# Kernel optimization log

Measured on AMD Instinct MI355X. Metric: run time of the kernel, lower is better.

## Reference

```python
import jax, jax.numpy as jnp
import numpy as np

N_NODES = 100000
N_EDGES = 500000
D = 256
EPS = 0.1  # GIN epsilon applied on self-loop relation


def setup_inputs() -> dict:
    key = jax.random.key(0)
    ks = jax.random.split(key, 9)
    return {
        "x": jax.random.normal(ks[0], (N_NODES, D), dtype=jnp.float32),
        "W_self": jax.random.normal(ks[1], (D, D), dtype=jnp.float32) * 0.05,
        "W_r1": jax.random.normal(ks[2], (D, D), dtype=jnp.float32) * 0.05,
        "W_r2": jax.random.normal(ks[3], (D, D), dtype=jnp.float32) * 0.05,
        "bias": jax.random.normal(ks[4], (D,), dtype=jnp.float32) * 0.05,
        "src1": jax.random.randint(ks[5], (N_EDGES,), 0, N_NODES, dtype=jnp.int32),
        "dst1": jax.random.randint(ks[6], (N_EDGES,), 0, N_NODES, dtype=jnp.int32),
        "src2": jax.random.randint(ks[7], (N_EDGES,), 0, N_NODES, dtype=jnp.int32),
        "dst2": jax.random.randint(ks[8], (N_EDGES,), 0, N_NODES, dtype=jnp.int32),
    }


def reference(x, W_self, W_r1, W_r2, bias, src1, dst1, src2, dst2):
    # self-loop relation: features scaled by (1+eps); one self-loop edge per node
    # so copy_u + sum delivers each node exactly its own message.
    h = (1.0 + EPS) * (x @ W_self)
    # regular relations: per-node message = x @ W, gathered along src edges,
    # scatter-summed at dst (DGL fn.copy_u + fn.sum, cross-etype 'sum' reducer).
    msg1 = x @ W_r1
    h = h + jax.ops.segment_sum(msg1[src1], dst1, num_segments=N_NODES)
    msg2 = x @ W_r2
    h = h + jax.ops.segment_sum(msg2[src2], dst2, num_segments=N_NODES)
    # bias + activation, then second activation (applied twice in original);
    # mlp/batch_norm are None, dropout is identity in eval.
    h = jax.nn.relu(h + bias)
    h = jax.nn.relu(h)
    return h
```

## Files before the change

kernel.cpp:

```cpp
#include <hip/hip_runtime.h>

#define N_NODES 100000
#define N_EDGES 500000
#define D 256
#define CAP 32

typedef __bf16 bf16x8 __attribute__((ext_vector_type(8)));
typedef float  f32x4  __attribute__((ext_vector_type(4)));

#define GLDS(gp, lp) \
    __builtin_amdgcn_global_load_lds((const __attribute__((address_space(1))) void*)(gp), \
                                     (__attribute__((address_space(3))) void*)(lp), 16, 0, 0)

__device__ __forceinline__ unsigned short f2bf(float f) {
    unsigned int u = __float_as_uint(f);
    u += 0x7fffu + ((u >> 16) & 1u);
    return (unsigned short)(u >> 16);
}
__device__ __forceinline__ float bf2f(unsigned short b) {
    return __uint_as_float(((unsigned int)b) << 16);
}

#define CONV_B   12500
#define PW_B     768
#define BKT_B    3907
#define PREP_GRID (CONV_B + PW_B + BKT_B)

__global__ __launch_bounds__(256) void prep_kernel(
    const float* __restrict__ x, unsigned short* __restrict__ xb,
    const float* __restrict__ Ws, const float* __restrict__ W1,
    const float* __restrict__ W2, unsigned short* __restrict__ Wt,
    const int* __restrict__ src1, const int* __restrict__ dst1,
    const int* __restrict__ src2, const int* __restrict__ dst2,
    int* __restrict__ cnt1, int* __restrict__ cnt2,
    int* __restrict__ bkt1, int* __restrict__ bkt2)
{
    const int b = blockIdx.x;
    const int tid = threadIdx.x;
    if (b < CONV_B) {
        size_t i = ((size_t)b * 256 + tid) * 8;
        if (i >= (size_t)N_NODES * D) return;
        float4 a = *(const float4*)(x + i);
        float4 c = *(const float4*)(x + i + 4);
        union { unsigned short s[8]; uint4 u; } o;
        o.s[0] = f2bf(a.x); o.s[1] = f2bf(a.y); o.s[2] = f2bf(a.z); o.s[3] = f2bf(a.w);
        o.s[4] = f2bf(c.x); o.s[5] = f2bf(c.y); o.s[6] = f2bf(c.z); o.s[7] = f2bf(c.w);
        *(uint4*)(xb + i) = o.u;
    } else if (b < CONV_B + PW_B) {
        int idx = (b - CONV_B) * 256 + tid;
        int k = idx >> 8;
        int n = idx & (D - 1);
        const float* W = (k < D) ? Ws : (k < 2 * D ? W1 : W2);
        float scale = (k < D) ? 1.1f : 1.0f;
        Wt[(size_t)n * (3 * D) + k] = f2bf(W[(size_t)(k & (D - 1)) * D + n] * scale);
    } else {
        int e = (b - CONV_B - PW_B) * 256 + tid;
        if (e >= 2 * N_EDGES) return;
        const int* src; const int* dst; int* cnt; int* bkt; int ei;
        if (e < N_EDGES) { src = src1; dst = dst1; cnt = cnt1; bkt = bkt1; ei = e; }
        else             { src = src2; dst = dst2; cnt = cnt2; bkt = bkt2; ei = e - N_EDGES; }
        int s = src[ei], d = dst[ei];
        int pos = atomicAdd(&cnt[d], 1);
        if (pos < CAP) bkt[d * CAP + pos] = s;
    }
}

__global__ __launch_bounds__(256) void gather_kernel(
    const unsigned short* __restrict__ xb,
    const int* __restrict__ cnt1, const int* __restrict__ cnt2,
    const int* __restrict__ bkt1, const int* __restrict__ bkt2,
    unsigned short* __restrict__ xa1, unsigned short* __restrict__ xa2)
{
    long long gid = (long long)blockIdx.x * blockDim.x + threadIdx.x;
    int node = (int)(gid >> 6);
    int lane = (int)(gid & 63);
    if (node >= N_NODES) return;

    int c1 = cnt1[node]; if (c1 > CAP) c1 = CAP;
    int c2 = cnt2[node]; if (c2 > CAP) c2 = CAP;

    int sid1 = (lane < c1) ? bkt1[(size_t)node * CAP + lane] : 0;
    int sid2 = (lane < c2) ? bkt2[(size_t)node * CAP + lane] : 0;

    ushort4 v1[8], v2[8];
    #pragma unroll
    for (int t = 0; t < 8; ++t) {
        int s = __shfl(sid1, t);
        v1[t] = *(const ushort4*)(xb + (size_t)s * D + lane * 4);
    }
    #pragma unroll
    for (int t = 0; t < 8; ++t) {
        int s = __shfl(sid2, t);
        v2[t] = *(const ushort4*)(xb + (size_t)s * D + lane * 4);
    }

    float a10 = 0.f, a11 = 0.f, a12 = 0.f, a13 = 0.f;
    float a20 = 0.f, a21 = 0.f, a22 = 0.f, a23 = 0.f;
    #pragma unroll
    for (int t = 0; t < 8; ++t) {
        if (t < c1) {
            a10 += bf2f(v1[t].x); a11 += bf2f(v1[t].y);
            a12 += bf2f(v1[t].z); a13 += bf2f(v1[t].w);
        }
        if (t < c2) {
            a20 += bf2f(v2[t].x); a21 += bf2f(v2[t].y);
            a22 += bf2f(v2[t].z); a23 += bf2f(v2[t].w);
        }
    }
    for (int e = 8; e < c1; ++e) {
        int s = __shfl(sid1, e);
        ushort4 v = *(const ushort4*)(xb + (size_t)s * D + lane * 4);
        a10 += bf2f(v.x); a11 += bf2f(v.y); a12 += bf2f(v.z); a13 += bf2f(v.w);
    }
    for (int e = 8; e < c2; ++e) {
        int s = __shfl(sid2, e);
        ushort4 v = *(const ushort4*)(xb + (size_t)s * D + lane * 4);
        a20 += bf2f(v.x); a21 += bf2f(v.y); a22 += bf2f(v.z); a23 += bf2f(v.w);
    }

    ushort4 o1, o2;
    o1.x = f2bf(a10); o1.y = f2bf(a11); o1.z = f2bf(a12); o1.w = f2bf(a13);
    o2.x = f2bf(a20); o2.y = f2bf(a21); o2.z = f2bf(a22); o2.w = f2bf(a23);
    *(ushort4*)(xa1 + (size_t)node * D + lane * 4) = o1;
    *(ushort4*)(xa2 + (size_t)node * D + lane * 4) = o2;
}

__global__ __launch_bounds__(512) void gemm_kernel(
    const unsigned short* __restrict__ xb,
    const unsigned short* __restrict__ xa1,
    const unsigned short* __restrict__ xa2,
    const unsigned short* __restrict__ Wt,
    const float* __restrict__ bias, float* __restrict__ out)
{
    __shared__ unsigned short Alds[128 * 32];
    __shared__ unsigned short Blds[256 * 32];

    const int tid  = threadIdx.x;
    const int lane = tid & 63;
    const int wave = tid >> 6;
    const int quad = lane >> 4;
    const int l15  = lane & 15;
    const int m0 = blockIdx.x * 128;
    const int wm = (wave >> 2) * 64;
    const int wn = (wave & 3) * 64;

    const unsigned short* Aseg[3] = {xb, xa1, xa2};

    f32x4 acc[4][4] = {};

    for (int kt = 0; kt < 24; ++kt) {
        const int seg = kt >> 3;
        const int ko  = (kt & 7) * 32;
        const unsigned short* __restrict__ A = Aseg[seg];

        {
            int row = tid >> 2, kq = tid & 3;
            int m = m0 + row;
            if (m >= N_NODES) m = N_NODES - 1;
            GLDS(A + (size_t)m * D + ko + kq * 8, Alds + tid * 8);
        }
        {
            int n = tid >> 2, kq = tid & 3;
            GLDS(Wt + (size_t)n * (3 * D) + kt * 32 + kq * 8, Blds + tid * 8);
        }
        {
            int t2 = tid + 512;
            int n = t2 >> 2, kq = t2 & 3;
            GLDS(Wt + (size_t)n * (3 * D) + kt * 32 + kq * 8, Blds + t2 * 8);
        }
        __syncthreads();

        bf16x8 af[4], bfr[4];
        #pragma unroll
        for (int i = 0; i < 4; ++i) {
            af[i]  = *(const bf16x8*)(Alds + (wm + i * 16 + l15) * 32 + quad * 8);
            bfr[i] = *(const bf16x8*)(Blds + (wn + i * 16 + l15) * 32 + quad * 8);
        }
        #pragma unroll
        for (int i = 0; i < 4; ++i)
            #pragma unroll
            for (int j = 0; j < 4; ++j)
                acc[i][j] = __builtin_amdgcn_mfma_f32_16x16x32_bf16(
                    af[i], bfr[j], acc[i][j], 0, 0, 0);
        __syncthreads();
    }

    #pragma unroll
    for (int j = 0; j < 4; ++j) {
        int col = wn + j * 16 + l15;
        float bj = bias[col];
        #pragma unroll
        for (int i = 0; i < 4; ++i) {
            int rb = m0 + wm + i * 16 + quad * 4;
            #pragma unroll
            for (int r = 0; r < 4; ++r) {
                int m = rb + r;
                if (m < N_NODES)
                    out[(size_t)m * D + col] = fmaxf(acc[i][j][r] + bj, 0.f);
            }
        }
    }
}

extern "C" void kernel_launch(void* const* d_in, const int* in_sizes, int n_in,
                              void* d_out, int out_size, void* d_ws, size_t ws_size,
                              hipStream_t stream) {
    const float* x    = (const float*)d_in[0];
    const float* Ws   = (const float*)d_in[1];
    const float* W1   = (const float*)d_in[2];
    const float* W2   = (const float*)d_in[3];
    const float* bias = (const float*)d_in[4];
    const int* src1   = (const int*)d_in[5];
    const int* dst1   = (const int*)d_in[6];
    const int* src2   = (const int*)d_in[7];
    const int* dst2   = (const int*)d_in[8];
    float* out = (float*)d_out;

    char* p = (char*)d_ws;
    unsigned short* xb  = (unsigned short*)p; p += (size_t)N_NODES * D * 2;
    unsigned short* xa1 = (unsigned short*)p; p += (size_t)N_NODES * D * 2;
    unsigned short* xa2 = (unsigned short*)p; p += (size_t)N_NODES * D * 2;
    int* cnt1 = (int*)p; p += (size_t)N_NODES * 4;
    int* cnt2 = (int*)p; p += (size_t)N_NODES * 4;
    int* bkt1 = (int*)p; p += (size_t)N_NODES * CAP * 4;
    int* bkt2 = (int*)p; p += (size_t)N_NODES * CAP * 4;
    unsigned short* Wt = (unsigned short*)p;

    hipMemsetAsync(cnt1, 0, (size_t)2 * N_NODES * 4, stream);

    prep_kernel<<<PREP_GRID, 256, 0, stream>>>(
        x, xb, Ws, W1, W2, Wt, src1, dst1, src2, dst2, cnt1, cnt2, bkt1, bkt2);

    {
        long long total = (long long)N_NODES * 64;
        gather_kernel<<<(int)((total + 255) / 256), 256, 0, stream>>>(
            xb, cnt1, cnt2, bkt1, bkt2, xa1, xa2);
    }
    {
        gemm_kernel<<<(N_NODES + 127) / 128, 512, 0, stream>>>(
            xb, xa1, xa2, Wt, bias, out);
    }
}
```

Before: 446.8 us.

## Interleave prep work per wave, split gather by relation, use nontemporal stores

The prep kernel now assigns work per wave in interleaved groups of 22 (16 convert, 5 bucket, 1 weight-transpose waves), so the bandwidth-bound conversion overlaps with the latency-bound atomic bucketing instead of running them as separate block ranges. The gather kernel launches one wave per (node, relation) pair instead of one per node, doubling the wave count and halving per-wave registers to raise occupancy and memory-level parallelism. Stores of the aggregated features and of the final output use nontemporal hints to reduce cache pollution. The costs are more total waves doing the same index loads, and nontemporal writes for xa1/xa2 may evict data the gemm would otherwise find in cache.

After: 403.9 us. 9.6% less time.

```diff
diff --git a/kernel.cpp b/kernel.cpp
--- a/kernel.cpp
+++ b/kernel.cpp
@@ -7,6 +7,7 @@
 
 typedef __bf16 bf16x8 __attribute__((ext_vector_type(8)));
 typedef float  f32x4  __attribute__((ext_vector_type(4)));
+typedef unsigned int u32x2 __attribute__((ext_vector_type(2)));
 
 #define GLDS(gp, lp) \
     __builtin_amdgcn_global_load_lds((const __attribute__((address_space(1))) void*)(gp), \
@@ -21,10 +22,7 @@
     return __uint_as_float(((unsigned int)b) << 16);
 }
 
-#define CONV_B   12500
-#define PW_B     768
-#define BKT_B    3907
-#define PREP_GRID (CONV_B + PW_B + BKT_B)
+#define PREP_BLOCKS 17188
 
 __global__ __launch_bounds__(256) void prep_kernel(
     const float* __restrict__ x, unsigned short* __restrict__ xb,
@@ -35,33 +33,42 @@
     int* __restrict__ cnt1, int* __restrict__ cnt2,
     int* __restrict__ bkt1, int* __restrict__ bkt2)
 {
-    const int b = blockIdx.x;
-    const int tid = threadIdx.x;
-    if (b < CONV_B) {
-        size_t i = ((size_t)b * 256 + tid) * 8;
-        if (i >= (size_t)N_NODES * D) return;
+    const int wid  = blockIdx.x * 4 + (threadIdx.x >> 6);
+    const int lane = threadIdx.x & 63;
+    const int group = wid / 22;
+    const int pos   = wid - group * 22;
+
+    if (pos < 16) {
+        int cw = group * 16 + pos;
+        if (cw >= 50000) return;
+        size_t i = (size_t)cw * 512 + (size_t)lane * 8;
         float4 a = *(const float4*)(x + i);
         float4 c = *(const float4*)(x + i + 4);
         union { unsigned short s[8]; uint4 u; } o;
         o.s[0] = f2bf(a.x); o.s[1] = f2bf(a.y); o.s[2] = f2bf(a.z); o.s[3] = f2bf(a.w);
         o.s[4] = f2bf(c.x); o.s[5] = f2bf(c.y); o.s[6] = f2bf(c.z); o.s[7] = f2bf(c.w);
         *(uint4*)(xb + i) = o.u;
-    } else if (b < CONV_B + PW_B) {
-        int idx = (b - CONV_B) * 256 + tid;
+    } else if (pos < 21) {
+        int bw = group * 5 + (pos - 16);
+        int e = bw * 64 + lane;
+        if (e >= 2 * N_EDGES) return;
+        bool r2 = (e >= N_EDGES);
+        const int* src = r2 ? src2 : src1;
+        const int* dst = r2 ? dst2 : dst1;
+        int* cnt = r2 ? cnt2 : cnt1;
+        int* bkt = r2 ? bkt2 : bkt1;
+        int ei = r2 ? e - N_EDGES : e;
+        int s = src[ei], d = dst[ei];
+        int p = atomicAdd(&cnt[d], 1);
+        if (p < CAP) bkt[d * CAP + p] = s;
+    } else {
+        int idx = group * 64 + lane;
+        if (idx >= 3 * D * D) return;
         int k = idx >> 8;
         int n = idx & (D - 1);
         const float* W = (k < D) ? Ws : (k < 2 * D ? W1 : W2);
         float scale = (k < D) ? 1.1f : 1.0f;
         Wt[(size_t)n * (3 * D) + k] = f2bf(W[(size_t)(k & (D - 1)) * D + n] * scale);
-    } else {
-        int e = (b - CONV_B - PW_B) * 256 + tid;
-        if (e >= 2 * N_EDGES) return;
-        const int* src; const int* dst; int* cnt; int* bkt; int ei;
-        if (e < N_EDGES) { src = src1; dst = dst1; cnt = cnt1; bkt = bkt1; ei = e; }
-        else             { src = src2; dst = dst2; cnt = cnt2; bkt = bkt2; ei = e - N_EDGES; }
-        int s = src[ei], d = dst[ei];
-        int pos = atomicAdd(&cnt[d], 1);
-        if (pos < CAP) bkt[d * CAP + pos] = s;
     }
 }
 
@@ -72,57 +79,44 @@
     unsigned short* __restrict__ xa1, unsigned short* __restrict__ xa2)
 {
     long long gid = (long long)blockIdx.x * blockDim.x + threadIdx.x;
-    int node = (int)(gid >> 6);
+    int w = (int)(gid >> 6);
     int lane = (int)(gid & 63);
-    if (node >= N_NODES) return;
-
-    int c1 = cnt1[node]; if (c1 > CAP) c1 = CAP;
-    int c2 = cnt2[node]; if (c2 > CAP) c2 = CAP;
-
-    int sid1 = (lane < c1) ? bkt1[(size_t)node * CAP + lane] : 0;
-    int sid2 = (lane < c2) ? bkt2[(size_t)node * CAP + lane] : 0;
-
-    ushort4 v1[8], v2[8];
+    if (w >= 2 * N_NODES) return;
+    int node = w >> 1;
+    int rel  = w & 1;
+
+    const int* cnt = rel ? cnt2 : cnt1;
+    const int* bkt = rel ? bkt2 : bkt1;
+    unsigned short* xa = rel ? xa2 : xa1;
+
+    int c = cnt[node]; if (c > CAP) c = CAP;
+    int sid = (lane < c) ? bkt[(size_t)node * CAP + lane] : 0;
+
+    ushort4 v[8];
     #pragma unroll
     for (int t = 0; t < 8; ++t) {
-        int s = __shfl(sid1, t);
-        v1[t] = *(const ushort4*)(xb + (size_t)s * D + lane * 4);
-    }
+        int s = __shfl(sid, t);
+        v[t] = *(const ushort4*)(xb + (size_t)s * D + lane * 4);
+    }
+
+    float a0 = 0.f, a1 = 0.f, a2 = 0.f, a3 = 0.f;
     #pragma unroll
     for (int t = 0; t < 8; ++t) {
-        int s = __shfl(sid2, t);
-        v2[t] = *(const ushort4*)(xb + (size_t)s * D + lane * 4);
-    }
-
-    float a10 = 0.f, a11 = 0.f, a12 = 0.f, a13 = 0.f;
-    float a20 = 0.f, a21 = 0.f, a22 = 0.f, a23 = 0.f;
-    #pragma unroll
-    for (int t = 0; t < 8; ++t) {
-        if (t < c1) {
-            a10 += bf2f(v1[t].x); a11 += bf2f(v1[t].y);
-            a12 += bf2f(v1[t].z); a13 += bf2f(v1[t].w);
-        }
-        if (t < c2) {
-            a20 += bf2f(v2[t].x); a21 += bf2f(v2[t].y);
-            a22 += bf2f(v2[t].z); a23 += bf2f(v2[t].w);
-        }
-    }
-    for (int e = 8; e < c1; ++e) {
-        int s = __shfl(sid1, e);
-        ushort4 v = *(const ushort4*)(xb + (size_t)s * D + lane * 4);
-        a10 += bf2f(v.x); a11 += bf2f(v.y); a12 += bf2f(v.z); a13 += bf2f(v.w);
-    }
-    for (int e = 8; e < c2; ++e) {
-        int s = __shfl(sid2, e);
-        ushort4 v = *(const ushort4*)(xb + (size_t)s * D + lane * 4);
-        a20 += bf2f(v.x); a21 += bf2f(v.y); a22 += bf2f(v.z); a23 += bf2f(v.w);
-    }
-
-    ushort4 o1, o2;
-    o1.x = f2bf(a10); o1.y = f2bf(a11); o1.z = f2bf(a12); o1.w = f2bf(a13);
-    o2.x = f2bf(a20); o2.y = f2bf(a21); o2.z = f2bf(a22); o2.w = f2bf(a23);
-    *(ushort4*)(xa1 + (size_t)node * D + lane * 4) = o1;
-    *(ushort4*)(xa2 + (size_t)node * D + lane * 4) = o2;
+        if (t < c) {
+            a0 += bf2f(v[t].x); a1 += bf2f(v[t].y);
+            a2 += bf2f(v[t].z); a3 += bf2f(v[t].w);
+        }
+    }
+    for (int e = 8; e < c; ++e) {
+        int s = __shfl(sid, e);
+        ushort4 t = *(const ushort4*)(xb + (size_t)s * D + lane * 4);
+        a0 += bf2f(t.x); a1 += bf2f(t.y); a2 += bf2f(t.z); a3 += bf2f(t.w);
+    }
+
+    u32x2 o;
+    o.x = (unsigned)f2bf(a0) | ((unsigned)f2bf(a1) << 16);
+    o.y = (unsigned)f2bf(a2) | ((unsigned)f2bf(a3) << 16);
+    __builtin_nontemporal_store(o, (u32x2*)(xa + (size_t)node * D + lane * 4));
 }
 
 __global__ __launch_bounds__(512) void gemm_kernel(
@@ -196,7 +190,9 @@
             for (int r = 0; r < 4; ++r) {
                 int m = rb + r;
                 if (m < N_NODES)
-                    out[(size_t)m * D + col] = fmaxf(acc[i][j][r] + bj, 0.f);
+                    __builtin_nontemporal_store(
+                        fmaxf(acc[i][j][r] + bj, 0.f),
+                        out + (size_t)m * D + col);
             }
         }
     }
@@ -226,13 +222,13 @@
     int* bkt2 = (int*)p; p += (size_t)N_NODES * CAP * 4;
     unsigned short* Wt = (unsigned short*)p;
 
-    hipMemsetAsync(cnt1, 0, (size_t)2 * N_NODES * 4, stream);
-
-    prep_kernel<<<PREP_GRID, 256, 0, stream>>>(
+    (void)hipMemsetAsync(cnt1, 0, (size_t)2 * N_NODES * 4, stream);
+
+    prep_kernel<<<PREP_BLOCKS, 256, 0, stream>>>(
         x, xb, Ws, W1, W2, Wt, src1, dst1, src2, dst2, cnt1, cnt2, bkt1, bkt2);
 
     {
-        long long total = (long long)N_NODES * 64;
+        long long total = (long long)2 * N_NODES * 64;
         gather_kernel<<<(int)((total + 255) / 256), 256, 0, stream>>>(
             xb, cnt1, cnt2, bkt1, bkt2, xa1, xa2);
     }
```
